# Kernel optimization log

Measured on AMD Instinct MI355X. Metric: run time of the kernel, lower is better.

The kernel has to match this reference:

```python
import jax, jax.numpy as jnp
import numpy as np
import math

EMBED_DIM = 256
SEQ_LEN = 4096
BATCH = 4
NUM_SCALES = (24.0, 720.0)


def setup_inputs() -> dict:
    key = jax.random.key(0)
    ks = jax.random.split(key, 8)
    d = EMBED_DIM
    x = jax.random.normal(ks[0], (BATCH, SEQ_LEN, d), dtype=jnp.float32)
    # nn.Linear params: weight [out, in], bias [out]
    s = 1.0 / math.sqrt(d)
    Wq = jax.random.uniform(ks[1], (d, d), jnp.float32, -s, s)
    bq = jax.random.uniform(ks[2], (d,), jnp.float32, -s, s)
    Wk = jax.random.uniform(ks[3], (d, d), jnp.float32, -s, s)
    bk = jax.random.uniform(ks[4], (d,), jnp.float32, -s, s)
    Wv = jax.random.uniform(ks[5], (d, d), jnp.float32, -s, s)
    bv = jax.random.uniform(ks[6], (d,), jnp.float32, -s, s)
    beta = jnp.ones((len(NUM_SCALES),), dtype=jnp.float32)
    return {"x": x, "Wq": Wq, "bq": bq, "Wk": Wk, "bk": bk, "Wv": Wv, "bv": bv, "beta": beta}


def reference(x, Wq, bq, Wk, bk, Wv, bv, beta):
    d = x.shape[-1]
    seq_len = x.shape[1]
    sqrt_d = jnp.asarray(math.sqrt(d), x.dtype)
    # Linear: y = x @ W^T + b
    Q = jnp.einsum('bsd,ed->bse', x, Wq) + bq
    K = jnp.einsum('bsd,ed->bse', x, Wk) + bk
    V = jnp.einsum('bsd,ed->bse', x, Wv) + bv
    attn = jnp.einsum('bse,bte->bst', Q, K) / sqrt_d  # [B,S,S]
    # multi-scale periodic bias (batch-independent): sum_n beta[n]*cos(2*pi*|i-j|/T_n)
    idx = jnp.arange(seq_len, dtype=jnp.float32)
    absdiff = jnp.abs(idx[:, None] - idx[None, :])  # [S,S]
    two_pi = jnp.asarray(2.0 * math.pi, jnp.float32)
    bias = jnp.zeros((seq_len, seq_len), dtype=jnp.float32)
    for n, T in enumerate(NUM_SCALES):
        bias = bias + beta[n] * jnp.cos(two_pi * absdiff / T)
    scores = jax.nn.softmax(attn + bias[None, :, :], axis=-1)
    return jnp.einsum('bst,bte->bse', scores, V)
```

## Files before the change

kernel.cpp:

```cpp
#include <hip/hip_runtime.h>
#include <math.h>
#include <stdint.h>

#define DEV static __device__ __forceinline__
typedef unsigned short u16;

constexpr int D = 256;
constexpr int S = 4096;
constexpr int QSTR = 272;
constexpr int KT_TILE = 8960;
constexpr int VT_TILE = 10240;

typedef short bf16x8 __attribute__((ext_vector_type(8)));
typedef float f32x16 __attribute__((ext_vector_type(16)));

DEV u16 f2bf(float f){ __bf16 b = (__bf16)f; return __builtin_bit_cast(u16, b); }
DEV float bf2f(u16 h){ return __uint_as_float(((unsigned)h)<<16); }
DEV int packbf(float lo, float hi){ return (int)((((unsigned)f2bf(hi)) << 16) | (unsigned)f2bf(lo)); }
DEV float bfsum2(int d){
  return __uint_as_float(((unsigned)d)<<16) + __uint_as_float(((unsigned)d) & 0xffff0000u);
}
DEV float ex2(float x){ return __builtin_amdgcn_exp2f(x); }
DEV void gl_lds16(const u16* g, u16* l) {
  __builtin_amdgcn_global_load_lds(
      (const __attribute__((address_space(1))) unsigned int*)g,
      (__attribute__((address_space(3))) unsigned int*)l, 16, 0, 0);
}

DEV void softmax_pf(const f32x16& s, int h, float& l_acc, bf16x8* pf) {
  #pragma unroll
  for (int s2 = 0; s2 < 2; ++s2) {
    float e0 = ex2(s[8*s2+0]), e1 = ex2(s[8*s2+1]);
    float e2 = ex2(s[8*s2+2]), e3 = ex2(s[8*s2+3]);
    float e4 = ex2(s[8*s2+4]), e5 = ex2(s[8*s2+5]);
    float e6 = ex2(s[8*s2+6]), e7 = ex2(s[8*s2+7]);
    int P0d0 = packbf(e0, e1), P0d1 = packbf(e2, e3);
    int P1d0 = packbf(e4, e5), P1d1 = packbf(e6, e7);
    l_acc += bfsum2(P0d0) + bfsum2(P0d1) + bfsum2(P1d0) + bfsum2(P1d1);
    int s0 = h ? P0d0 : P1d0;
    int s1 = h ? P0d1 : P1d1;
    int r0 = __shfl_xor(s0, 32, 64);
    int r1 = __shfl_xor(s1, 32, 64);
    union { int d[4]; bf16x8 v; } u;
    u.d[0] = h ? r0 : P0d0;
    u.d[1] = h ? r1 : P0d1;
    u.d[2] = h ? P1d0 : r0;
    u.d[3] = h ? P1d1 : r1;
    pf[s2] = u.v;
  }
}

__global__ __launch_bounds__(256) void msp_prep(
    const float* __restrict__ x, const float* __restrict__ Wq,
    const float* __restrict__ Wk, const float* __restrict__ Wv,
    const float* __restrict__ beta,
    u16* __restrict__ xc, u16* __restrict__ Wc,
    u16* __restrict__ Qb, u16* __restrict__ Kt,
    float* __restrict__ Lacc)
{
  const int blk = blockIdx.x, tid = threadIdx.x;
  if (blk < 2048) {
    int row = blk*8 + (tid>>5);
    int col = (tid&31)*8;
    const float* p = x + (size_t)row*256 + col;
    union { u16 s[8]; uint4 v; } hh, ll;
    #pragma unroll
    for (int i=0;i<8;++i){ float v = p[i]; u16 h2 = f2bf(v); hh.s[i]=h2; ll.s[i]=f2bf(v - bf2f(h2)); }
    *(uint4*)(xc + (size_t)row*512 + col)       = hh.v;
    *(uint4*)(xc + (size_t)row*512 + 256 + col) = ll.v;
  } else if (blk < 2144) {
    int q = blk - 2048;
    int mat = q >> 5;
    int idx = (q & 31)*2048 + tid*8;
    int o = idx >> 8, cc = idx & 255;
    const float* W = mat==0 ? Wq : (mat==1 ? Wk : Wv);
    float sc = (mat==0) ? 0.09016844005556021f : 1.0f;
    const float* p = W + (size_t)o*256 + cc;
    union { u16 s[8]; uint4 v; } hh, ll;
    #pragma unroll
    for (int i=0;i<8;++i){ float v = p[i]*sc; u16 h2 = f2bf(v); hh.s[i]=h2; ll.s[i]=f2bf(v - bf2f(h2)); }
    *(uint4*)(Wc + (size_t)(mat*256 + o)*512 + cc)       = hh.v;
    *(uint4*)(Wc + (size_t)(mat*256 + o)*512 + 256 + cc) = ll.v;
  } else if (blk < 2208) {
    int row = (blk - 2144)*256 + tid;
    int s = row & (S-1);
    int bb = row >> 12;
    constexpr float L2E = 1.4426950408889634f;
    float b0 = beta[0]*L2E, b1 = beta[1]*L2E;
    int i24 = s % 24, i720 = s % 720;
    float t0 = (float)i24  * 0.26179938779914944f;
    float t1 = (float)i720 * 0.008726646259971648f;
    float c0 = cosf(t0), s0 = sinf(t0), c1 = cosf(t1), s1 = sinf(t1);
    float qv[4] = {b0*c0, b0*s0, b1*c1, b1*s1};
    float kv[4] = {c0, s0, c1, s1};
    u16* qp = Qb + (size_t)row*QSTR + 256;
    u16* kp = Kt + (size_t)(bb*128 + (s>>5))*KT_TILE + (s&31)*280 + 256;
    #pragma unroll
    for (int n=0;n<4;++n){
      u16 uh = f2bf(qv[n]); u16 ul = f2bf(qv[n]-bf2f(uh));
      u16 vh = f2bf(kv[n]); u16 vl = f2bf(kv[n]-bf2f(vh));
      qp[n*3+0]=uh; qp[n*3+1]=uh; qp[n*3+2]=ul;
      kp[n*3+0]=vh; kp[n*3+1]=vl; kp[n*3+2]=vh;
    }
    #pragma unroll
    for (int c=12;c<16;++c){ qp[c]=0; kp[c]=0; }
  } else {
    float4* p = (float4*)Lacc;
    float4 z = {0.f,0.f,0.f,0.f};
    #pragma unroll
    for (int c=0;c<16;++c) p[tid + c*256] = z;
  }
}

__global__ __launch_bounds__(256, 2) void msp_proj(
    const u16* __restrict__ xc, const u16* __restrict__ Wc,
    const float* __restrict__ bq, const float* __restrict__ bk, const float* __restrict__ bv,
    u16* __restrict__ Qb, u16* __restrict__ Kt, u16* __restrict__ Vt)
{
  __shared__ __align__(16) u16 smem[2][2][128][72];

  const int tid = threadIdx.x;
  const int w = tid >> 6, lane = tid & 63;
  const int l31 = lane & 31, h = lane >> 5;
  const int m0 = blockIdx.x * 128;
  const int nblk = blockIdx.y;
  const int n0 = nblk * 128, mat = nblk >> 1, cb = (nblk & 1) * 128;
  const int mh = (w & 1) * 64, nh = (w >> 1) * 64;

  const int srow = tid & 127;
  const int isB = tid >> 7;
  const u16* sgbase = isB ? (Wc + (size_t)(n0 + srow)*512) : (xc + (size_t)(m0 + srow)*512);

  {
    u16* d = &smem[0][isB][srow][0];
    #pragma unroll
    for (int jj=0; jj<8; ++jj) *(uint4*)(d + jj*8) = *(const uint4*)(sgbase + jj*8);
  }

  f32x16 acc[2][2];
  #pragma unroll
  for (int a=0;a<2;++a)
    #pragma unroll
    for (int c=0;c<2;++c)
      #pragma unroll
      for (int i=0;i<16;++i) acc[a][c][i] = 0.f;

  for (int kc8 = 0; kc8 < 8; ++kc8) {
    __syncthreads();
    const int p = kc8 & 1;
    uint4 nxt[8];
    if (kc8 < 7) {
      const u16* g = sgbase + (kc8+1)*64;
      #pragma unroll
      for (int jj=0; jj<8; ++jj) nxt[jj] = *(const uint4*)(g + jj*8);
    }
    #pragma unroll
    for (int kf = 0; kf < 4; ++kf) {
      const int ko = kf*16 + h*8;
      bf16x8 a0 = *(const bf16x8*)&smem[p][0][mh + l31][ko];
      bf16x8 a1 = *(const bf16x8*)&smem[p][0][mh + 32 + l31][ko];
      bf16x8 b0 = *(const bf16x8*)&smem[p][1][nh + l31][ko];
      bf16x8 b1 = *(const bf16x8*)&smem[p][1][nh + 32 + l31][ko];
      acc[0][0] = __builtin_amdgcn_mfma_f32_32x32x16_bf16(a0, b0, acc[0][0], 0,0,0);
      acc[0][1] = __builtin_amdgcn_mfma_f32_32x32x16_bf16(a0, b1, acc[0][1], 0,0,0);
      acc[1][0] = __builtin_amdgcn_mfma_f32_32x32x16_bf16(a1, b0, acc[1][0], 0,0,0);
      acc[1][1] = __builtin_amdgcn_mfma_f32_32x32x16_bf16(a1, b1, acc[1][1], 0,0,0);
    }
    if (kc8 < 7) {
      u16* d = &smem[p^1][isB][srow][0];
      #pragma unroll
      for (int jj=0; jj<8; ++jj) *(uint4*)(d + jj*8) = nxt[jj];
    }
  }

  const float* bias = mat==0 ? bq : (mat==1 ? bk : bv);
  const float bsc = (mat==0) ? 0.09016844005556021f : 1.0f;
  float bb_[2];
  #pragma unroll
  for (int ntl=0; ntl<2; ++ntl) bb_[ntl] = bias[cb + nh + ntl*32 + l31] * bsc;

  if (mat <= 1) {
    #pragma unroll
    for (int mt=0; mt<2; ++mt)
      #pragma unroll
      for (int ntl=0; ntl<2; ++ntl)
        #pragma unroll
        for (int r=0; r<16; ++r) {
          int gm = m0 + mh + mt*32 + (r&3) + 8*(r>>2) + 4*h;
          int col = cb + nh + ntl*32 + l31;
          u16 val = f2bf(acc[mt][ntl][r] + bb_[ntl]);
          if (mat == 0) {
            Qb[(size_t)gm*QSTR + col] = val;
          } else {
            int bb2 = gm >> 12, s = gm & (S-1);
            Kt[(size_t)(bb2*128 + (s>>5))*KT_TILE + (s&31)*280 + col] = val;
          }
        }
  } else {
    u16* T = (u16*)smem;
    #pragma unroll
    for (int mt=0; mt<2; ++mt)
      #pragma unroll
      for (int ntl=0; ntl<2; ++ntl)
        #pragma unroll
        for (int r=0; r<16; ++r) {
          int e_loc = nh + ntl*32 + l31;
          int m_loc = mh + mt*32 + (r&3) + 8*(r>>2) + 4*h;
          T[(size_t)e_loc*136 + m_loc] = f2bf(acc[mt][ntl][r] + bb_[ntl]);
        }
    __syncthreads();
    int e_loc = tid >> 1, shalf = (tid & 1)*64;
    int e = cb + e_loc;
    #pragma unroll
    for (int g2 = 0; g2 < 2; ++g2) {
      int gm = m0 + shalf + g2*32;
      int bb2 = gm >> 12, s = gm & (S-1);
      u16* dst = Vt + (size_t)(bb2*128 + (s>>5))*VT_TILE + (size_t)e*40;
      const u16* src = T + (size_t)e_loc*136 + shalf + g2*32;
      #pragma unroll
      for (int k2=0;k2<4;++k2) *(uint4*)(dst + k2*8) = *(const uint4*)(src + k2*8);
    }
  }
}

__global__ __launch_bounds__(256, 2) void msp_attn(
    const u16* __restrict__ Qb, const u16* __restrict__ Kt,
    const u16* __restrict__ Vt, float* __restrict__ out,
    float* __restrict__ P1, float* __restrict__ P23,
    float* __restrict__ Lacc)
{
  __shared__ __align__(16) unsigned char smem[77824];

  const int tid = threadIdx.x;
  const int w = tid >> 6, lane = tid & 63;
  const int l31 = lane & 31, h = lane >> 5;

  const int xg = blockIdx.x;
  const int xcd = xg & 7, j = xg >> 3;
  const int c = xcd*2 + (j & 1);
  const int qt = j >> 1;
  const int b = c >> 2, tq = c & 3;
  const int q0 = qt * 128;
  const int qw = q0 + w*32;

  bf16x8 qf[17];
  {
    const u16* qp = Qb + ((size_t)b*S + qw + l31)*QSTR + h*8;
    #pragma unroll
    for (int s2=0; s2<17; ++s2) qf[s2] = *(const bf16x8*)(qp + s2*16);
  }

  const int tIdx0 = b*128 + tq*32;

  f32x16 oacc[8];
  #pragma unroll
  for (int e=0;e<8;++e)
    #pragma unroll
    for (int i=0;i<16;++i) oacc[e][i] = 0.f;
  float l_acc = 0.f;

  {
    const u16* kg = Kt + (size_t)tIdx0*KT_TILE;
    u16* kl = (u16*)smem;
    #pragma unroll
    for (int i = w; i < 18; i += 4) gl_lds16(kg + i*512 + lane*8, kl + i*512);
  }

  bf16x8 pf[2];

  {
    __syncthreads();
    const u16* kg = Kt + (size_t)(tIdx0 + 1)*KT_TILE;
    u16* kl = (u16*)(smem + 18432);
    #pragma unroll
    for (int i = w; i < 18; i += 4) gl_lds16(kg + i*512 + lane*8, kl + i*512);
    const u16* vg = Vt + (size_t)tIdx0*VT_TILE;
    u16* vl = (u16*)(smem + 36864);
    #pragma unroll
    for (int i = w; i < 20; i += 4) gl_lds16(vg + i*512 + lane*8, vl + i*512);

    const u16* Kp = (const u16*)smem + (size_t)l31*280 + h*8;
    f32x16 sa;
    #pragma unroll
    for (int i=0;i<16;++i) sa[i] = 0.f;
    __builtin_amdgcn_s_setprio(1);
    #pragma unroll
    for (int s2 = 0; s2 < 17; ++s2) {
      bf16x8 kf = *(const bf16x8*)(Kp + s2*16);
      sa = __builtin_amdgcn_mfma_f32_32x32x16_bf16(kf, qf[s2], sa, 0,0,0);
    }
    __builtin_amdgcn_s_setprio(0);
    softmax_pf(sa, h, l_acc, pf);
  }

  for (int it = 1; it < 32; ++it) {
    const int p = it & 1;
    __syncthreads();

    if (it < 31) {
      const u16* kg = Kt + (size_t)(tIdx0 + it + 1)*KT_TILE;
      u16* kl = (u16*)(smem + (p^1)*18432);
      #pragma unroll
      for (int i = w; i < 18; i += 4) gl_lds16(kg + i*512 + lane*8, kl + i*512);
    }
    {
      const u16* vg = Vt + (size_t)(tIdx0 + it)*VT_TILE;
      u16* vl = (u16*)(smem + 36864 + p*20480);
      #pragma unroll
      for (int i = w; i < 20; i += 4) gl_lds16(vg + i*512 + lane*8, vl + i*512);
    }

    const u16* Kp = (const u16*)(smem + p*18432) + (size_t)l31*280 + h*8;
    const u16* Vp = (const u16*)(smem + 36864 + (p^1)*20480) + (size_t)l31*40 + h*8;
    f32x16 sa;
    #pragma unroll
    for (int i=0;i<16;++i) sa[i] = 0.f;
    __builtin_amdgcn_s_setprio(1);
    #pragma unroll
    for (int s2 = 0; s2 < 17; ++s2) {
      bf16x8 kf = *(const bf16x8*)(Kp + s2*16);
      sa = __builtin_amdgcn_mfma_f32_32x32x16_bf16(kf, qf[s2], sa, 0,0,0);
      if (s2 < 16) {
        const u16* vb = Vp + (s2>>1)*(32*40) + (s2&1)*16;
        oacc[s2>>1] = __builtin_amdgcn_mfma_f32_32x32x16_bf16(*(const bf16x8*)vb, pf[s2&1], oacc[s2>>1], 0,0,0);
      }
    }
    __builtin_amdgcn_s_setprio(0);

    softmax_pf(sa, h, l_acc, pf);
  }

  float l_tot = l_acc + __shfl_xor(l_acc, 32, 64);
  if (h == 0) unsafeAtomicAdd(&Lacc[(size_t)b*S + qw + l31], l_tot);

  __syncthreads();
  {
    const u16* Vp = (const u16*)(smem + 36864 + 20480) + (size_t)l31*40 + h*8;
    __builtin_amdgcn_s_setprio(1);
    #pragma unroll
    for (int et = 0; et < 8; ++et) {
      const u16* vb = Vp + et*32*40;
      oacc[et] = __builtin_amdgcn_mfma_f32_32x32x16_bf16(*(const bf16x8*)(vb),      pf[0], oacc[et], 0,0,0);
      oacc[et] = __builtin_amdgcn_mfma_f32_32x32x16_bf16(*(const bf16x8*)(vb + 16), pf[1], oacc[et], 0,0,0);
    }
    __builtin_amdgcn_s_setprio(0);
  }

  float* dst = (tq == 0) ? (out + (size_t)b*S*D)
             : (tq == 1) ? (P1 + (size_t)b*S*D)
                         : (P23 + ((size_t)(tq-2)*4 + b)*S*D);
  float* OflA = (float*)smem;
  float* OflB = (float*)smem + 8320;
  for (int rr = 0; rr < 2; ++rr) {
    __syncthreads();
    if ((w >> 1) == rr) {
      float* Of = (w & 1) ? OflB : OflA;
      #pragma unroll
      for (int et=0; et<8; ++et)
        #pragma unroll
        for (int g=0; g<4; ++g) {
          float4 v4 = { oacc[et][4*g+0], oacc[et][4*g+1], oacc[et][4*g+2], oacc[et][4*g+3] };
          *(float4*)&Of[(size_t)l31*260 + et*32 + 8*g + 4*h] = v4;
        }
    }
    __syncthreads();
    #pragma unroll
    for (int hf = 0; hf < 2; ++hf) {
      const float* Of = hf ? OflB : OflA;
      float* obase = dst + (size_t)(q0 + (rr*2 + hf)*32)*D;
      #pragma unroll
      for (int q2 = 0; q2 < 8; ++q2) {
        int q = q2*4 + (tid>>6);
        int e4 = (tid & 63)*4;
        *(float4*)(obase + (size_t)q*D + e4) = *(const float4*)&Of[(size_t)q*260 + e4];
      }
    }
  }
}

__global__ __launch_bounds__(256) void msp_norm(
    float* __restrict__ out, const float* __restrict__ P1,
    const float* __restrict__ P23, const float* __restrict__ L)
{
  constexpr size_t PSZ = (size_t)4*S*D;
  int idx = blockIdx.x*256 + threadIdx.x;
  int row = idx >> 6, e0 = (idx & 63)*4;
  size_t off = (size_t)row*256 + e0;
  float inv = 1.0f / L[row];
  float4 v  = *(const float4*)(out + off);
  float4 a  = *(const float4*)(P1  + off);
  float4 b2 = *(const float4*)(P23 + off);
  float4 c2 = *(const float4*)(P23 + PSZ + off);
  v.x = (v.x + a.x + b2.x + c2.x) * inv;
  v.y = (v.y + a.y + b2.y + c2.y) * inv;
  v.z = (v.z + a.z + b2.z + c2.z) * inv;
  v.w = (v.w + a.w + b2.w + c2.w) * inv;
  *(float4*)(out + off) = v;
}

extern "C" void kernel_launch(void* const* d_in, const int* in_sizes, int n_in,
                              void* d_out, int out_size, void* d_ws, size_t ws_size,
                              hipStream_t stream) {
  const float* x    = (const float*)d_in[0];
  const float* Wq   = (const float*)d_in[1];
  const float* bq   = (const float*)d_in[2];
  const float* Wk   = (const float*)d_in[3];
  const float* bk   = (const float*)d_in[4];
  const float* Wv   = (const float*)d_in[5];
  const float* bv   = (const float*)d_in[6];
  const float* beta = (const float*)d_in[7];
  float* out = (float*)d_out;

  char* w = (char*)d_ws;
  u16* xc = (u16*)w;
  float* P1 = (float*)w;
  w += (size_t)16384*512*2;
  u16* Wc = (u16*)w;  w += (size_t)768*512*2;
  u16* Qb = (u16*)w;  w += (size_t)16384*QSTR*2;
  u16* Kt = (u16*)w;  w += (size_t)512*KT_TILE*2;
  u16* Vt = (u16*)w;  w += (size_t)512*VT_TILE*2;
  float* Lacc = (float*)w; w += (size_t)16384*4;
  float* P23 = (float*)w;

  msp_prep<<<2209, 256, 0, stream>>>(x, Wq, Wk, Wv, beta, xc, Wc, Qb, Kt, Lacc);
  msp_proj<<<dim3(128, 6), 256, 0, stream>>>(xc, Wc, bq, bk, bv, Qb, Kt, Vt);
  msp_attn<<<512, 256, 0, stream>>>(Qb, Kt, Vt, out, P1, P23, Lacc);
  msp_norm<<<4096, 256, 0, stream>>>(out, P1, P23, Lacc);
}
```

Baseline: 203.5 us.

## Pre-tile projection operands in XOR-swizzled chunk layout and load via direct-to-LDS

The prep kernel now writes the bf16 hi/lo split of x and the weights in a blocked, chunk-major layout with an XOR swizzle per row. The projection kernel then streams each K-chunk straight into LDS with global_load_lds instead of staging through registers, and reads fragments through the matching swizzle, so the padded LDS rows are no longer needed. This is meant to cut register pressure and VGPR round trips and to avoid LDS bank conflicts in the projection GEMM. The price is coupling between the prep layout and the consumer, plus an extra barrier before the V transpose reuses shared memory.

```diff
diff --git a/kernel.cpp b/kernel.cpp
--- a/kernel.cpp
+++ b/kernel.cpp
@@ -25,6 +25,13 @@
   __builtin_amdgcn_global_load_lds(
       (const __attribute__((address_space(1))) unsigned int*)g,
       (__attribute__((address_space(3))) unsigned int*)l, 16, 0, 0);
+}
+
+DEV size_t cm_addr(int rowblock, int chunk, int row_in, int j) {
+  return ((size_t)rowblock*8 + chunk)*8192 + (size_t)(((row_in<<3) + j) ^ (row_in & 7))*8;
+}
+DEV const u16* swz(const u16* base, int row, int slot) {
+  return base + ((((row<<3) + slot) ^ (row & 7)) << 3);
 }
 
 DEV void softmax_pf(const f32x16& s, int h, float& l_acc, bf16x8* pf) {
@@ -66,8 +73,10 @@
     union { u16 s[8]; uint4 v; } hh, ll;
     #pragma unroll
     for (int i=0;i<8;++i){ float v = p[i]; u16 h2 = f2bf(v); hh.s[i]=h2; ll.s[i]=f2bf(v - bf2f(h2)); }
-    *(uint4*)(xc + (size_t)row*512 + col)       = hh.v;
-    *(uint4*)(xc + (size_t)row*512 + 256 + col) = ll.v;
+    int rb = row >> 7, rin = row & 127;
+    int ch = col >> 6, j = (col >> 3) & 7;
+    *(uint4*)(xc + cm_addr(rb, ch,     rin, j)) = hh.v;
+    *(uint4*)(xc + cm_addr(rb, ch + 4, rin, j)) = ll.v;
   } else if (blk < 2144) {
     int q = blk - 2048;
     int mat = q >> 5;
@@ -79,8 +88,11 @@
     union { u16 s[8]; uint4 v; } hh, ll;
     #pragma unroll
     for (int i=0;i<8;++i){ float v = p[i]*sc; u16 h2 = f2bf(v); hh.s[i]=h2; ll.s[i]=f2bf(v - bf2f(h2)); }
-    *(uint4*)(Wc + (size_t)(mat*256 + o)*512 + cc)       = hh.v;
-    *(uint4*)(Wc + (size_t)(mat*256 + o)*512 + 256 + cc) = ll.v;
+    int rowg = mat*256 + o;
+    int rb = rowg >> 7, rin = rowg & 127;
+    int ch = cc >> 6, j = (cc >> 3) & 7;
+    *(uint4*)(Wc + cm_addr(rb, ch,     rin, j)) = hh.v;
+    *(uint4*)(Wc + cm_addr(rb, ch + 4, rin, j)) = ll.v;
   } else if (blk < 2208) {
     int row = (blk - 2144)*256 + tid;
     int s = row & (S-1);
@@ -117,24 +129,24 @@
     const float* __restrict__ bq, const float* __restrict__ bk, const float* __restrict__ bv,
     u16* __restrict__ Qb, u16* __restrict__ Kt, u16* __restrict__ Vt)
 {
-  __shared__ __align__(16) u16 smem[2][2][128][72];
+  __shared__ __align__(16) u16 smem[2][2][128][64];
 
   const int tid = threadIdx.x;
   const int w = tid >> 6, lane = tid & 63;
   const int l31 = lane & 31, h = lane >> 5;
   const int m0 = blockIdx.x * 128;
   const int nblk = blockIdx.y;
-  const int n0 = nblk * 128, mat = nblk >> 1, cb = (nblk & 1) * 128;
+  const int mat = nblk >> 1, cb = (nblk & 1) * 128;
   const int mh = (w & 1) * 64, nh = (w >> 1) * 64;
 
-  const int srow = tid & 127;
-  const int isB = tid >> 7;
-  const u16* sgbase = isB ? (Wc + (size_t)(n0 + srow)*512) : (xc + (size_t)(m0 + srow)*512);
+  const u16* Ag = xc + (size_t)blockIdx.x*8*8192;
+  const u16* Bg = Wc + (size_t)nblk*8*8192;
 
   {
-    u16* d = &smem[0][isB][srow][0];
-    #pragma unroll
-    for (int jj=0; jj<8; ++jj) *(uint4*)(d + jj*8) = *(const uint4*)(sgbase + jj*8);
+    #pragma unroll
+    for (int i = w; i < 16; i += 4) gl_lds16(Ag + i*512 + lane*8, &smem[0][0][0][0] + i*512);
+    #pragma unroll
+    for (int i = w; i < 16; i += 4) gl_lds16(Bg + i*512 + lane*8, &smem[0][1][0][0] + i*512);
   }
 
   f32x16 acc[2][2];
@@ -148,28 +160,27 @@
   for (int kc8 = 0; kc8 < 8; ++kc8) {
     __syncthreads();
     const int p = kc8 & 1;
-    uint4 nxt[8];
     if (kc8 < 7) {
-      const u16* g = sgbase + (kc8+1)*64;
-      #pragma unroll
-      for (int jj=0; jj<8; ++jj) nxt[jj] = *(const uint4*)(g + jj*8);
-    }
+      const u16* a2 = Ag + (size_t)(kc8+1)*8192;
+      const u16* b2 = Bg + (size_t)(kc8+1)*8192;
+      #pragma unroll
+      for (int i = w; i < 16; i += 4) gl_lds16(a2 + i*512 + lane*8, &smem[p^1][0][0][0] + i*512);
+      #pragma unroll
+      for (int i = w; i < 16; i += 4) gl_lds16(b2 + i*512 + lane*8, &smem[p^1][1][0][0] + i*512);
+    }
+    const u16* As = &smem[p][0][0][0];
+    const u16* Bs = &smem[p][1][0][0];
     #pragma unroll
     for (int kf = 0; kf < 4; ++kf) {
-      const int ko = kf*16 + h*8;
-      bf16x8 a0 = *(const bf16x8*)&smem[p][0][mh + l31][ko];
-      bf16x8 a1 = *(const bf16x8*)&smem[p][0][mh + 32 + l31][ko];
-      bf16x8 b0 = *(const bf16x8*)&smem[p][1][nh + l31][ko];
-      bf16x8 b1 = *(const bf16x8*)&smem[p][1][nh + 32 + l31][ko];
+      const int slot = kf*2 + h;
+      bf16x8 a0 = *(const bf16x8*)swz(As, mh + l31, slot);
+      bf16x8 a1 = *(const bf16x8*)swz(As, mh + 32 + l31, slot);
+      bf16x8 b0 = *(const bf16x8*)swz(Bs, nh + l31, slot);
+      bf16x8 b1 = *(const bf16x8*)swz(Bs, nh + 32 + l31, slot);
       acc[0][0] = __builtin_amdgcn_mfma_f32_32x32x16_bf16(a0, b0, acc[0][0], 0,0,0);
       acc[0][1] = __builtin_amdgcn_mfma_f32_32x32x16_bf16(a0, b1, acc[0][1], 0,0,0);
       acc[1][0] = __builtin_amdgcn_mfma_f32_32x32x16_bf16(a1, b0, acc[1][0], 0,0,0);
       acc[1][1] = __builtin_amdgcn_mfma_f32_32x32x16_bf16(a1, b1, acc[1][1], 0,0,0);
-    }
-    if (kc8 < 7) {
-      u16* d = &smem[p^1][isB][srow][0];
-      #pragma unroll
-      for (int jj=0; jj<8; ++jj) *(uint4*)(d + jj*8) = nxt[jj];
     }
   }
 
@@ -197,6 +208,7 @@
           }
         }
   } else {
+    __syncthreads();
     u16* T = (u16*)smem;
     #pragma unroll
     for (int mt=0; mt<2; ++mt)
```

Measured after the change: 192.9 us. 1.05x faster.
